# Performance work log

Hardware: AMD Instinct MI355X
Metric: run time of the kernel (lower is better)

Reference implementation:

```python
import jax, jax.numpy as jnp
import numpy as np

N_DIM = 768
HIDDEN_DIM = 768
BATCH = 4
SEQ = 2048


def setup_inputs() -> dict:
    key = jax.random.key(0)
    ks = jax.random.split(key, 9)
    s_in = 1.0 / np.sqrt(N_DIM)
    s_h = 1.0 / np.sqrt(HIDDEN_DIM)
    return {
        "x": jax.random.normal(ks[0], (BATCH, SEQ, N_DIM), dtype=jnp.float32),
        # torch Linear weights: [out_features, in_features]
        "wq": jax.random.uniform(ks[1], (HIDDEN_DIM, N_DIM), jnp.float32, -s_in, s_in),
        "bq": jax.random.uniform(ks[2], (HIDDEN_DIM,), jnp.float32, -s_in, s_in),
        "wk": jax.random.uniform(ks[3], (HIDDEN_DIM, N_DIM), jnp.float32, -s_in, s_in),
        "bk": jax.random.uniform(ks[4], (HIDDEN_DIM,), jnp.float32, -s_in, s_in),
        "wv": jax.random.uniform(ks[5], (HIDDEN_DIM, N_DIM), jnp.float32, -s_in, s_in),
        "bv": jax.random.uniform(ks[6], (HIDDEN_DIM,), jnp.float32, -s_in, s_in),
        "wo": jax.random.uniform(ks[7], (N_DIM, HIDDEN_DIM), jnp.float32, -s_h, s_h),
        "bo": jax.random.uniform(ks[8], (N_DIM,), jnp.float32, -s_h, s_h),
    }


def reference(x, wq, bq, wk, bk, wv, bv, wo, bo):
    # q,k,v: [B, S, H]
    q = jnp.einsum("bsd,hd->bsh", x, wq) + bq
    k = jnp.einsum("bsd,hd->bsh", x, wk) + bk
    v = jnp.einsum("bsd,hd->bsh", x, wv) + bv
    # NOTE: faithful to source — no 1/sqrt(d) scaling, no mask.
    scores = jnp.einsum("bqh,bkh->bqk", q, k)  # [B, S, S]
    attn = jax.nn.softmax(scores, axis=-1)
    y = jnp.einsum("bqk,bkh->bqh", attn, v)  # [B, S, H]
    out = jnp.einsum("bsh,dh->bsd", y, wo) + bo
    return out
```

## Files before the change

kernel.cpp:

```cpp
#include <hip/hip_runtime.h>

typedef _Float16 f16;
typedef _Float16 f16x8 __attribute__((ext_vector_type(8)));
typedef float f32x4 __attribute__((ext_vector_type(4)));

#define GLD16(g, l) __builtin_amdgcn_global_load_lds( \
    (const __attribute__((address_space(1))) void*)(g), \
    (__attribute__((address_space(3))) void*)(l), 16, 0, 0)

template <typename OutT, int BM, int BN, int MODE, int MINW>
__global__ __launch_bounds__(256, MINW)
void gemm_kernel(const f16* __restrict__ A, long sA,
                 const f16* __restrict__ B, long sB,
                 void* __restrict__ Cv, long sC,
                 void* __restrict__ C2v,
                 const float* __restrict__ bias,
                 const float* __restrict__ bias2,
                 int N, int K)
{
    constexpr int FM = BM / 32;
    constexpr int FN = BN / 32;
    constexpr int IA = BM / 32;
    constexpr int IB = BN / 32;

    OutT* C  = (OutT*)Cv;
    OutT* C2 = (OutT*)C2v;
    const int tid  = threadIdx.x;
    const int wave = tid >> 6;
    const int lane = tid & 63;
    const int bz   = blockIdx.z;
    A += (long)bz * sA;
    B += (long)bz * sB;
    C += (long)bz * sC;
    const long bm = (long)blockIdx.x * BM;
    const long bn = (long)blockIdx.y * BN;

    __shared__ f16 sAt[BM * 64];
    __shared__ f16 sBt[BN * 64];

    const int srow = lane >> 3;
    const int gch  = ((lane & 7) ^ srow) * 8;

    const f16* gAb = A + (bm + wave * (BM / 4) + srow) * (long)K + gch;
    const f16* gBb = B + (bn + wave * (BN / 4) + srow) * (long)K + gch;

    const int wm = (wave >> 1) * (BM / 2);
    const int wn = (wave & 1) * (BN / 2);
    const int lr = lane & 15;
    const int qd = lane >> 4;
    const int swz0 = ((0 * 4 + qd) ^ (lr & 7)) * 8;
    const int swz1 = ((1 * 4 + qd) ^ (lr & 7)) * 8;

    f32x4 acc[FM][FN] = {};

    for (int k0 = 0; k0 < K; k0 += 64) {
        #pragma unroll
        for (int i = 0; i < IA; ++i)
            GLD16(gAb + k0 + (long)i * 8 * K, &sAt[(wave * (BM / 4) + i * 8) * 64]);
        #pragma unroll
        for (int i = 0; i < IB; ++i)
            GLD16(gBb + k0 + (long)i * 8 * K, &sBt[(wave * (BN / 4) + i * 8) * 64]);
        __syncthreads();

        #pragma unroll
        for (int h = 0; h < 2; ++h) {
            const int swz = h ? swz1 : swz0;
            f16x8 af[FM], bf[FN];
            #pragma unroll
            for (int t = 0; t < FM; ++t)
                af[t] = *(const f16x8*)&sAt[(wm + t * 16 + lr) * 64 + swz];
            #pragma unroll
            for (int t = 0; t < FN; ++t)
                bf[t] = *(const f16x8*)&sBt[(wn + t * 16 + lr) * 64 + swz];
            #pragma unroll
            for (int tm = 0; tm < FM; ++tm)
                #pragma unroll
                for (int tn = 0; tn < FN; ++tn)
                    acc[tm][tn] = __builtin_amdgcn_mfma_f32_16x16x32_f16(
                        af[tm], bf[tn], acc[tm][tn], 0, 0, 0);
        }
        __syncthreads();
    }

    #pragma unroll
    for (int tn = 0; tn < FN; ++tn) {
        const long col = bn + wn + tn * 16 + lr;
        OutT* dst = C;
        long cc = col, stride = N;
        float bc = 0.f;
        if (MODE == 1) bc = bias[col];
        if (MODE == 3) {
            stride = 768;
            if (col >= 768) { dst = C2; cc = col - 768; bc = bias2[cc]; }
            else            { bc = bias[cc]; }
        }
        #pragma unroll
        for (int tm = 0; tm < FM; ++tm) {
            #pragma unroll
            for (int r = 0; r < 4; ++r) {
                const long row = bm + wm + tm * 16 + qd * 4 + r;
                float v = acc[tm][tn][r] + bc;
                if (MODE == 2) v += bias[row];
                dst[row * stride + cc] = (OutT)v;
            }
        }
    }
}

__global__ __launch_bounds__(256)
void softmax_kernel(f16* __restrict__ S)
{
    const long row = blockIdx.x;
    f16* p = S + row * 2048;
    const int tid  = threadIdx.x;
    const int wave = tid >> 6;
    const int lane = tid & 63;

    f16x8 x = *(const f16x8*)&p[tid * 8];
    float v[8];
    float m = -1e30f;
    #pragma unroll
    for (int j = 0; j < 8; ++j) { v[j] = (float)x[j]; m = fmaxf(m, v[j]); }
    #pragma unroll
    for (int off = 32; off > 0; off >>= 1) m = fmaxf(m, __shfl_down(m, off));

    __shared__ float rm[4], rs[4];
    if (lane == 0) rm[wave] = m;
    __syncthreads();
    m = fmaxf(fmaxf(rm[0], rm[1]), fmaxf(rm[2], rm[3]));

    float s = 0.f;
    #pragma unroll
    for (int j = 0; j < 8; ++j) { v[j] = __expf(v[j] - m); s += v[j]; }
    #pragma unroll
    for (int off = 32; off > 0; off >>= 1) s += __shfl_down(s, off);
    if (lane == 0) rs[wave] = s;
    __syncthreads();
    s = rs[0] + rs[1] + rs[2] + rs[3];
    const float inv = 1.0f / s;

    f16x8 y;
    #pragma unroll
    for (int j = 0; j < 8; ++j) y[j] = (f16)(v[j] * inv);
    *(f16x8*)&p[tid * 8] = y;
}

__global__ __launch_bounds__(256)
void cvt_all_kernel(const float* __restrict__ x,
                    const float* __restrict__ w0, const float* __restrict__ w1,
                    const float* __restrict__ w2, const float* __restrict__ w3,
                    f16* __restrict__ x16, f16* __restrict__ w16)
{
    const float* in; f16* out; long i;
    if (blockIdx.x < 3072) {
        in = x; out = x16;
        i = ((long)blockIdx.x * 256 + threadIdx.x) * 8;
    } else {
        const int wb  = blockIdx.x - 3072;
        const int sel = wb / 288;
        in  = (sel == 0) ? w0 : (sel == 1) ? w1 : (sel == 2) ? w2 : w3;
        out = w16 + (long)sel * 589824;
        i = ((long)(wb - sel * 288) * 256 + threadIdx.x) * 8;
    }
    float4 a = *(const float4*)(in + i);
    float4 b = *(const float4*)(in + i + 4);
    f16x8 o;
    o[0] = (f16)a.x; o[1] = (f16)a.y; o[2] = (f16)a.z; o[3] = (f16)a.w;
    o[4] = (f16)b.x; o[5] = (f16)b.y; o[6] = (f16)b.z; o[7] = (f16)b.w;
    *(f16x8*)&out[i] = o;
}

__global__ __launch_bounds__(256)
void transpose_kernel(const f16* __restrict__ in, f16* __restrict__ out)
{
    __shared__ f16 t[64][72];
    const int r  = threadIdx.x >> 2;
    const int c0 = (threadIdx.x & 3) * 16;
    const f16* src = in + ((long)blockIdx.x * 64 + r) * 768 + blockIdx.y * 64 + c0;
    f16x8 a = *(const f16x8*)src;
    f16x8 b = *(const f16x8*)(src + 8);
    #pragma unroll
    for (int i = 0; i < 8; ++i) { t[r][c0 + i] = a[i]; t[r][c0 + 8 + i] = b[i]; }
    __syncthreads();
    f16x8 o1, o2;
    #pragma unroll
    for (int i = 0; i < 8; ++i) { o1[i] = t[c0 + i][r]; o2[i] = t[c0 + 8 + i][r]; }
    f16* dst = out + ((long)blockIdx.y * 64 + r) * 768 + blockIdx.x * 64 + c0;
    *(f16x8*)dst = o1;
    *(f16x8*)(dst + 8) = o2;
}

__global__ __launch_bounds__(256)
void wobv_kernel(const float* __restrict__ wo, const float* __restrict__ bv,
                 float* __restrict__ c)
{
    const int d = blockIdx.x;
    const int tid = threadIdx.x;
    float s = 0.f;
    for (int h = tid; h < 768; h += 256) s += wo[d * 768 + h] * bv[h];
    #pragma unroll
    for (int off = 32; off > 0; off >>= 1) s += __shfl_down(s, off);
    __shared__ float rs[4];
    if ((tid & 63) == 0) rs[tid >> 6] = s;
    __syncthreads();
    if (tid == 0) c[d] = rs[0] + rs[1] + rs[2] + rs[3];
}

extern "C" void kernel_launch(void* const* d_in, const int* in_sizes, int n_in,
                              void* d_out, int out_size, void* d_ws, size_t ws_size,
                              hipStream_t stream)
{
    const float* x  = (const float*)d_in[0];
    const float* wq = (const float*)d_in[1];
    const float* bq = (const float*)d_in[2];
    const float* wk = (const float*)d_in[3];
    const float* bk = (const float*)d_in[4];
    const float* wv = (const float*)d_in[5];
    const float* bv = (const float*)d_in[6];
    const float* wo = (const float*)d_in[7];
    const float* bo = (const float*)d_in[8];

    char* ws = (char*)d_ws;
    f16* x16  = (f16*)(ws + 0);
    f16* w16  = (f16*)(ws + 12582912);
    f16* Q    = (f16*)(ws + 17301504);
    f16* Kb   = (f16*)(ws + 29884416);
    f16* VWT  = (f16*)(ws + 42467328);
    f16* S    = (f16*)(ws + 55050240);
    f16* wvT  = (f16*)(ws + 88604672);
    f16* Wc   = (f16*)(ws + 89784320);
    float* cB = (float*)(ws + 90963968);

    f16* wv16 = w16 + 2 * 589824;
    f16* wo16 = w16 + 3 * 589824;

    cvt_all_kernel<<<4224, 256, 0, stream>>>(x, wq, wk, wv, wo, x16, w16);

    transpose_kernel<<<dim3(12, 12), 256, 0, stream>>>(wv16, wvT);
    wobv_kernel<<<768, 256, 0, stream>>>(wo, bv, cB);
    gemm_kernel<f16, 128, 128, 0, 3><<<dim3(6, 6, 1), 256, 0, stream>>>(
        wo16, 0, wvT, 0, Wc, 0, nullptr, nullptr, nullptr, 768, 768);

    gemm_kernel<f16, 128, 128, 3, 3><<<dim3(64, 12, 1), 256, 0, stream>>>(
        x16, 0, w16, 0, Q, 0, Kb, bq, bk, 1536, 768);
    gemm_kernel<f16, 64, 128, 2, 4><<<dim3(12, 16, 4), 256, 0, stream>>>(
        Wc, 0, x16, (long)2048 * 768, VWT, (long)768 * 2048, nullptr,
        cB, nullptr, 2048, 768);
    gemm_kernel<f16, 128, 256, 0, 2><<<dim3(16, 8, 4), 256, 0, stream>>>(
        Q, (long)2048 * 768, Kb, (long)2048 * 768, S, (long)2048 * 2048,
        nullptr, nullptr, nullptr, 2048, 768);
    softmax_kernel<<<8192, 256, 0, stream>>>(S);
    gemm_kernel<float, 128, 64, 1, 4><<<dim3(16, 12, 4), 256, 0, stream>>>(
        S, (long)2048 * 2048, VWT, (long)768 * 2048, d_out, (long)2048 * 768,
        nullptr, bo, nullptr, 768, 2048);
}
```

Measured before the change: 237.8 us.

## Fuse weight prep kernels into conversion launch and Wc GEMM into QK projection

The wv transpose and the wo·bv bias reduction move into the fp32-to-fp16 conversion kernel as extra block ranges. The wo·wvT product (Wc) now runs as an extra grid row of the Q/K projection GEMM instead of its own launch. Together this cuts the preprocessing chain from six launches to two and removes the serial dependency gaps between the small kernels. The risk is that the extra GEMM row adds tail blocks to the QK projection launch, and that the transpose now reads fp32 wv directly.

Result: faster. 228.0 us (-4.1%).

```diff
diff --git a/kernel.cpp b/kernel.cpp
--- a/kernel.cpp
+++ b/kernel.cpp
@@ -16,7 +16,10 @@
                  void* __restrict__ C2v,
                  const float* __restrict__ bias,
                  const float* __restrict__ bias2,
-                 int N, int K)
+                 int N, int K,
+                 const f16* __restrict__ A2,
+                 const f16* __restrict__ B2,
+                 void* __restrict__ C3v)
 {
     constexpr int FM = BM / 32;
     constexpr int FN = BN / 32;
@@ -29,11 +32,23 @@
     const int wave = tid >> 6;
     const int lane = tid & 63;
     const int bz   = blockIdx.z;
-    A += (long)bz * sA;
-    B += (long)bz * sB;
+
+    const f16* Ab = A + (long)bz * sA;
+    const f16* Bb = B + (long)bz * sB;
     C += (long)bz * sC;
-    const long bm = (long)blockIdx.x * BM;
-    const long bn = (long)blockIdx.y * BN;
+    int Kk = K;
+    long bm, bn;
+    bool sub = false;
+    if (MODE == 3 && blockIdx.y == gridDim.y - 1) {
+        if (blockIdx.x >= 36) return;
+        sub = true;
+        Ab = A2; Bb = B2; Kk = 768;
+        bm = (long)(blockIdx.x / 6) * BM;
+        bn = (long)(blockIdx.x % 6) * BN;
+    } else {
+        bm = (long)blockIdx.x * BM;
+        bn = (long)blockIdx.y * BN;
+    }
 
     __shared__ f16 sAt[BM * 64];
     __shared__ f16 sBt[BN * 64];
@@ -41,8 +56,8 @@
     const int srow = lane >> 3;
     const int gch  = ((lane & 7) ^ srow) * 8;
 
-    const f16* gAb = A + (bm + wave * (BM / 4) + srow) * (long)K + gch;
-    const f16* gBb = B + (bn + wave * (BN / 4) + srow) * (long)K + gch;
+    const f16* gAb = Ab + (bm + wave * (BM / 4) + srow) * (long)Kk + gch;
+    const f16* gBb = Bb + (bn + wave * (BN / 4) + srow) * (long)Kk + gch;
 
     const int wm = (wave >> 1) * (BM / 2);
     const int wn = (wave & 1) * (BN / 2);
@@ -53,13 +68,13 @@
 
     f32x4 acc[FM][FN] = {};
 
-    for (int k0 = 0; k0 < K; k0 += 64) {
+    for (int k0 = 0; k0 < Kk; k0 += 64) {
         #pragma unroll
         for (int i = 0; i < IA; ++i)
-            GLD16(gAb + k0 + (long)i * 8 * K, &sAt[(wave * (BM / 4) + i * 8) * 64]);
+            GLD16(gAb + k0 + (long)i * 8 * Kk, &sAt[(wave * (BM / 4) + i * 8) * 64]);
         #pragma unroll
         for (int i = 0; i < IB; ++i)
-            GLD16(gBb + k0 + (long)i * 8 * K, &sBt[(wave * (BN / 4) + i * 8) * 64]);
+            GLD16(gBb + k0 + (long)i * 8 * Kk, &sBt[(wave * (BN / 4) + i * 8) * 64]);
         __syncthreads();
 
         #pragma unroll
@@ -82,6 +97,21 @@
         __syncthreads();
     }
 
+    if (MODE == 3 && sub) {
+        f16* W = (f16*)C3v;
+        #pragma unroll
+        for (int tn = 0; tn < FN; ++tn) {
+            const long col = bn + wn + tn * 16 + lr;
+            #pragma unroll
+            for (int tm = 0; tm < FM; ++tm)
+                #pragma unroll
+                for (int r = 0; r < 4; ++r) {
+                    const long row = bm + wm + tm * 16 + qd * 4 + r;
+                    W[row * 768 + col] = (f16)acc[tm][tn][r];
+                }
+        }
+        return;
+    }
     #pragma unroll
     for (int tn = 0; tn < FN; ++tn) {
         const long col = bn + wn + tn * 16 + lr;
@@ -147,63 +177,80 @@
 
 __global__ __launch_bounds__(256)
 void cvt_all_kernel(const float* __restrict__ x,
-                    const float* __restrict__ w0, const float* __restrict__ w1,
-                    const float* __restrict__ w2, const float* __restrict__ w3,
-                    f16* __restrict__ x16, f16* __restrict__ w16)
-{
-    const float* in; f16* out; long i;
-    if (blockIdx.x < 3072) {
-        in = x; out = x16;
-        i = ((long)blockIdx.x * 256 + threadIdx.x) * 8;
+                    const float* __restrict__ wq, const float* __restrict__ wk,
+                    const float* __restrict__ wv, const float* __restrict__ wo,
+                    const float* __restrict__ bv,
+                    f16* __restrict__ x16, f16* __restrict__ w16,
+                    f16* __restrict__ wvT, float* __restrict__ cB)
+{
+    __shared__ f16 t[64][72];
+    const int b = blockIdx.x;
+    const int tid = threadIdx.x;
+
+    if (b < 3936) {
+        const float* in; f16* out; long i;
+        if (b < 3072) {
+            in = x; out = x16;
+            i = ((long)b * 256 + tid) * 8;
+        } else {
+            const int wb  = b - 3072;
+            const int sel = wb / 288;
+            in  = (sel == 0) ? wq : (sel == 1) ? wk : wo;
+            out = w16 + (long)((sel == 2) ? 3 : sel) * 589824;
+            i = ((long)(wb - sel * 288) * 256 + tid) * 8;
+        }
+        float4 a = *(const float4*)(in + i);
+        float4 c = *(const float4*)(in + i + 4);
+        f16x8 o;
+        o[0] = (f16)a.x; o[1] = (f16)a.y; o[2] = (f16)a.z; o[3] = (f16)a.w;
+        o[4] = (f16)c.x; o[5] = (f16)c.y; o[6] = (f16)c.z; o[7] = (f16)c.w;
+        *(f16x8*)&out[i] = o;
+    } else if (b < 4080) {
+        const int tb = b - 3936;
+        const int tr = tb / 12, tc = tb % 12;
+        const int r  = tid >> 2;
+        const int c0 = (tid & 3) * 16;
+        const float* src = wv + ((long)tr * 64 + r) * 768 + tc * 64 + c0;
+        float4 a0 = *(const float4*)(src);
+        float4 a1 = *(const float4*)(src + 4);
+        float4 a2 = *(const float4*)(src + 8);
+        float4 a3 = *(const float4*)(src + 12);
+        f16 vv[16];
+        vv[0]=(f16)a0.x; vv[1]=(f16)a0.y; vv[2]=(f16)a0.z; vv[3]=(f16)a0.w;
+        vv[4]=(f16)a1.x; vv[5]=(f16)a1.y; vv[6]=(f16)a1.z; vv[7]=(f16)a1.w;
+        vv[8]=(f16)a2.x; vv[9]=(f16)a2.y; vv[10]=(f16)a2.z; vv[11]=(f16)a2.w;
+        vv[12]=(f16)a3.x; vv[13]=(f16)a3.y; vv[14]=(f16)a3.z; vv[15]=(f16)a3.w;
+        f16* wv16 = w16 + (long)2 * 589824;
+        f16x8 o1, o2;
+        #pragma unroll
+        for (int i = 0; i < 8; ++i) { o1[i] = vv[i]; o2[i] = vv[8 + i]; }
+        f16* d16 = wv16 + ((long)tr * 64 + r) * 768 + tc * 64 + c0;
+        *(f16x8*)d16 = o1;
+        *(f16x8*)(d16 + 8) = o2;
+        #pragma unroll
+        for (int i = 0; i < 16; ++i) t[r][c0 + i] = vv[i];
+        __syncthreads();
+        #pragma unroll
+        for (int i = 0; i < 8; ++i) { o1[i] = t[c0 + i][r]; o2[i] = t[c0 + 8 + i][r]; }
+        f16* dT = wvT + ((long)tc * 64 + r) * 768 + tr * 64 + c0;
+        *(f16x8*)dT = o1;
+        *(f16x8*)(dT + 8) = o2;
     } else {
-        const int wb  = blockIdx.x - 3072;
-        const int sel = wb / 288;
-        in  = (sel == 0) ? w0 : (sel == 1) ? w1 : (sel == 2) ? w2 : w3;
-        out = w16 + (long)sel * 589824;
-        i = ((long)(wb - sel * 288) * 256 + threadIdx.x) * 8;
-    }
-    float4 a = *(const float4*)(in + i);
-    float4 b = *(const float4*)(in + i + 4);
-    f16x8 o;
-    o[0] = (f16)a.x; o[1] = (f16)a.y; o[2] = (f16)a.z; o[3] = (f16)a.w;
-    o[4] = (f16)b.x; o[5] = (f16)b.y; o[6] = (f16)b.z; o[7] = (f16)b.w;
-    *(f16x8*)&out[i] = o;
-}
-
-__global__ __launch_bounds__(256)
-void transpose_kernel(const f16* __restrict__ in, f16* __restrict__ out)
-{
-    __shared__ f16 t[64][72];
-    const int r  = threadIdx.x >> 2;
-    const int c0 = (threadIdx.x & 3) * 16;
-    const f16* src = in + ((long)blockIdx.x * 64 + r) * 768 + blockIdx.y * 64 + c0;
-    f16x8 a = *(const f16x8*)src;
-    f16x8 b = *(const f16x8*)(src + 8);
-    #pragma unroll
-    for (int i = 0; i < 8; ++i) { t[r][c0 + i] = a[i]; t[r][c0 + 8 + i] = b[i]; }
-    __syncthreads();
-    f16x8 o1, o2;
-    #pragma unroll
-    for (int i = 0; i < 8; ++i) { o1[i] = t[c0 + i][r]; o2[i] = t[c0 + 8 + i][r]; }
-    f16* dst = out + ((long)blockIdx.y * 64 + r) * 768 + blockIdx.x * 64 + c0;
-    *(f16x8*)dst = o1;
-    *(f16x8*)(dst + 8) = o2;
-}
-
-__global__ __launch_bounds__(256)
-void wobv_kernel(const float* __restrict__ wo, const float* __restrict__ bv,
-                 float* __restrict__ c)
-{
-    const int d = blockIdx.x;
-    const int tid = threadIdx.x;
-    float s = 0.f;
-    for (int h = tid; h < 768; h += 256) s += wo[d * 768 + h] * bv[h];
-    #pragma unroll
-    for (int off = 32; off > 0; off >>= 1) s += __shfl_down(s, off);
-    __shared__ float rs[4];
-    if ((tid & 63) == 0) rs[tid >> 6] = s;
-    __syncthreads();
-    if (tid == 0) c[d] = rs[0] + rs[1] + rs[2] + rs[3];
+        const int d0 = (b - 4080) * 64;
+        const int wave = tid >> 6, lane = tid & 63;
+        for (int it = 0; it < 16; ++it) {
+            const int d = d0 + it * 4 + wave;
+            float s = 0.f;
+            #pragma unroll
+            for (int j = 0; j < 12; ++j) {
+                const int h = lane + 64 * j;
+                s += wo[(long)d * 768 + h] * bv[h];
+            }
+            #pragma unroll
+            for (int off = 32; off > 0; off >>= 1) s += __shfl_down(s, off);
+            if (lane == 0) cB[d] = s;
+        }
+    }
 }
 
 extern "C" void kernel_launch(void* const* d_in, const int* in_sizes, int n_in,
@@ -231,26 +278,20 @@
     f16* Wc   = (f16*)(ws + 89784320);
     float* cB = (float*)(ws + 90963968);
 
-    f16* wv16 = w16 + 2 * 589824;
     f16* wo16 = w16 + 3 * 589824;
 
-    cvt_all_kernel<<<4224, 256, 0, stream>>>(x, wq, wk, wv, wo, x16, w16);
-
-    transpose_kernel<<<dim3(12, 12), 256, 0, stream>>>(wv16, wvT);
-    wobv_kernel<<<768, 256, 0, stream>>>(wo, bv, cB);
-    gemm_kernel<f16, 128, 128, 0, 3><<<dim3(6, 6, 1), 256, 0, stream>>>(
-        wo16, 0, wvT, 0, Wc, 0, nullptr, nullptr, nullptr, 768, 768);
-
-    gemm_kernel<f16, 128, 128, 3, 3><<<dim3(64, 12, 1), 256, 0, stream>>>(
-        x16, 0, w16, 0, Q, 0, Kb, bq, bk, 1536, 768);
+    cvt_all_kernel<<<4092, 256, 0, stream>>>(x, wq, wk, wv, wo, bv,
+                                             x16, w16, wvT, cB);
+    gemm_kernel<f16, 128, 128, 3, 3><<<dim3(64, 13, 1), 256, 0, stream>>>(
+        x16, 0, w16, 0, Q, 0, Kb, bq, bk, 1536, 768, wo16, wvT, Wc);
     gemm_kernel<f16, 64, 128, 2, 4><<<dim3(12, 16, 4), 256, 0, stream>>>(
         Wc, 0, x16, (long)2048 * 768, VWT, (long)768 * 2048, nullptr,
-        cB, nullptr, 2048, 768);
+        cB, nullptr, 2048, 768, nullptr, nullptr, nullptr);
     gemm_kernel<f16, 128, 256, 0, 2><<<dim3(16, 8, 4), 256, 0, stream>>>(
         Q, (long)2048 * 768, Kb, (long)2048 * 768, S, (long)2048 * 2048,
-        nullptr, nullptr, nullptr, 2048, 768);
+        nullptr, nullptr, nullptr, 2048, 768, nullptr, nullptr, nullptr);
     softmax_kernel<<<8192, 256, 0, stream>>>(S);
     gemm_kernel<float, 128, 64, 1, 4><<<dim3(16, 12, 4), 256, 0, stream>>>(
         S, (long)2048 * 2048, VWT, (long)768 * 2048, d_out, (long)2048 * 768,
-        nullptr, bo, nullptr, 768, 2048);
-}
+        nullptr, bo, nullptr, 768, 2048, nullptr, nullptr, nullptr);
+}
```
